# Optimization experiments

Hardware: AMD Instinct MI355X
Metric: run time of the kernel (lower is better)

The kernel has to match this reference:

```python
import jax, jax.numpy as jnp
import numpy as np

EPS = 1e-5

def _layernorm(h, g, b):
    mu = jnp.mean(h, axis=-1, keepdims=True)
    var = jnp.var(h, axis=-1, keepdims=True)
    return (h - mu) * jax.lax.rsqrt(var + EPS) * g + b

def setup_inputs() -> dict:
    key = jax.random.key(0)
    ks = jax.random.split(key, 12)
    N, D, E = 100000, 128, 1000000
    dims = [2 * D, 256, 128]  # [256, 256, 128]
    def lin(k, din, dout):
        s = 1.0 / np.sqrt(din)
        k1, k2 = jax.random.split(k)
        W = jax.random.uniform(k1, (din, dout), jnp.float32, -s, s)
        b = jax.random.uniform(k2, (dout,), jnp.float32, -s, s)
        return W, b
    x = jax.random.normal(ks[0], (N, D), jnp.float32)
    edge_index = jax.random.randint(ks[1], (2, E), 0, N, jnp.int32)
    w1, b1 = lin(ks[2], dims[0], dims[1])
    w2, b2 = lin(ks[3], dims[1], dims[2])
    wp, bp = lin(ks[4], dims[2], 1)
    ww, bw = lin(ks[5], dims[2], 1)
    return {
        "x": x, "edge_index": edge_index,
        "ln0_g": jnp.ones((dims[0],), jnp.float32), "ln0_b": jnp.zeros((dims[0],), jnp.float32),
        "w1": w1, "b1": b1,
        "ln1_g": jnp.ones((dims[1],), jnp.float32), "ln1_b": jnp.zeros((dims[1],), jnp.float32),
        "w2": w2, "b2": b2,
        "ln2_g": jnp.ones((dims[2],), jnp.float32), "ln2_b": jnp.zeros((dims[2],), jnp.float32),
        "wp": wp, "bp": bp, "ww": ww, "bw": bw,
    }

def reference(x, edge_index, ln0_g, ln0_b, w1, b1, ln1_g, ln1_b, w2, b2, ln2_g, ln2_b, wp, bp, ww, bw):
    src = x[edge_index[0]]          # [E, D] gather
    dst = x[edge_index[1]]          # [E, D] gather
    feats = jnp.concatenate([src + dst, src * dst], axis=-1)  # [E, 2D]
    h = _layernorm(feats, ln0_g, ln0_b)
    h = jax.nn.relu(_layernorm(h @ w1 + b1, ln1_g, ln1_b))
    h = jax.nn.relu(_layernorm(h @ w2 + b2, ln2_g, ln2_b))
    edge_probabilities = h @ wp + bp            # logits, [E, 1]
    edge_weights = jax.nn.relu(h @ ww + bw)     # [E, 1]
    return edge_probabilities, edge_weights
```

## Files before the change

kernel.cpp:

```cpp
#include <hip/hip_runtime.h>

#define EPS 1e-5f
#define PITCH 528

typedef __attribute__((ext_vector_type(8))) _Float16 f16x8;
typedef __attribute__((ext_vector_type(4))) _Float16 f16x4v;
typedef __attribute__((ext_vector_type(2))) _Float16 f16x2v;
typedef __attribute__((ext_vector_type(16))) float f32x16;

__global__ __launch_bounds__(256) void prep_x(const float* __restrict__ x,
                                              _Float16* __restrict__ x16, long n)
{
    const long i = ((long)blockIdx.x * 256 + threadIdx.x) * 8;
    if (i + 7 < n) {
        const float4 a = *reinterpret_cast<const float4*>(&x[i]);
        const float4 b = *reinterpret_cast<const float4*>(&x[i + 4]);
        f16x8 v;
        v[0] = (_Float16)a.x; v[1] = (_Float16)a.y; v[2] = (_Float16)a.z; v[3] = (_Float16)a.w;
        v[4] = (_Float16)b.x; v[5] = (_Float16)b.y; v[6] = (_Float16)b.z; v[7] = (_Float16)b.w;
        *reinterpret_cast<f16x8*>(&x16[i]) = v;
    }
}

__global__ __launch_bounds__(256) void prep_weights(
    const float* __restrict__ w1, const float* __restrict__ w2,
    _Float16* __restrict__ wb1, _Float16* __restrict__ wb2)
{
    const int t = blockIdx.x * 256 + threadIdx.x;
    const int lane = t & 63, frag = t >> 6;
    _Float16 v[8];
    if (frag < 128) {
        const int row0 = (frag & 15) * 16 + (lane >> 5) * 8;
        const int col = (frag >> 4) * 32 + (lane & 31);
        #pragma unroll
        for (int j = 0; j < 8; ++j) v[j] = (_Float16)w1[(row0 + j) * 256 + col];
        *reinterpret_cast<f16x8*>(&wb1[frag * 512 + lane * 8]) = *reinterpret_cast<f16x8*>(v);
    } else if (frag < 192) {
        const int f = frag - 128;
        const int row0 = (f & 15) * 16 + (lane >> 5) * 8;
        const int col = (f >> 4) * 32 + (lane & 31);
        #pragma unroll
        for (int j = 0; j < 8; ++j) v[j] = (_Float16)w2[(row0 + j) * 128 + col];
        *reinterpret_cast<f16x8*>(&wb2[f * 512 + lane * 8]) = *reinterpret_cast<f16x8*>(v);
    }
}

template<bool X16>
__global__ __launch_bounds__(1024, 4) void edge_mlp(
    const float* __restrict__ x, const _Float16* __restrict__ x16,
    const int* __restrict__ ei,
    const float* __restrict__ ln0_g, const float* __restrict__ ln0_b,
    const _Float16* __restrict__ wb1, const float* __restrict__ b1,
    const float* __restrict__ ln1_g, const float* __restrict__ ln1_b,
    const _Float16* __restrict__ wb2, const float* __restrict__ b2,
    const float* __restrict__ ln2_g, const float* __restrict__ ln2_b,
    const float* __restrict__ wp, const float* __restrict__ bp,
    const float* __restrict__ ww, const float* __restrict__ bw,
    float* __restrict__ out, int E)
{
    __shared__ __align__(16) _Float16 hh[128 * 264 + 8192];
    __shared__ __align__(8) float red[16][64][2];
    __shared__ __align__(8) float red2[16][32][2];

    const int tid = threadIdx.x, lane = tid & 63, w = tid >> 6;
    const int l31 = lane & 31, lh = lane >> 5;
    const int ft = w >> 1, ep = w & 1;
    const int ft2 = w >> 2, et2 = w & 3;
    const long base = (long)blockIdx.x * 128;

    {
        int si = 0;
        if (lane < 16) {
            const long idx = base + w * 8 + (lane >> 1);
            const int s = lane & 1;
            si = (idx < E) ? ei[(long)s * E + idx] : 0;
        }
        const int c = 2 * lane;
        const float ga = ln0_g[c], gb = ln0_g[c + 1], gc = ln0_g[128 + c], gd = ln0_g[129 + c];
        const float ba = ln0_b[c], bb = ln0_b[c + 1], bc = ln0_b[128 + c], bd = ln0_b[129 + c];
        char* hhc = (char*)hh;
        #pragma unroll
        for (int e8 = 0; e8 < 8; ++e8) {
            const int s0 = __shfl(si, e8 * 2 + 0);
            const int s1 = __shfl(si, e8 * 2 + 1);
            const int e = w * 8 + e8;
            float2 sv, dv;
            if constexpr (X16) {
                const f16x2v a2 = *reinterpret_cast<const f16x2v*>(&x16[(long)s0 * 128 + c]);
                const f16x2v d2 = *reinterpret_cast<const f16x2v*>(&x16[(long)s1 * 128 + c]);
                sv.x = (float)a2[0]; sv.y = (float)a2[1];
                dv.x = (float)d2[0]; dv.y = (float)d2[1];
            } else {
                sv = *reinterpret_cast<const float2*>(&x[(long)s0 * 128 + c]);
                dv = *reinterpret_cast<const float2*>(&x[(long)s1 * 128 + c]);
            }
            const float a0 = sv.x + dv.x, a1 = sv.y + dv.y;
            const float m0 = sv.x * dv.x, m1 = sv.y * dv.y;
            float s = a0 + a1 + m0 + m1;
            float q = a0 * a0 + a1 * a1 + m0 * m0 + m1 * m1;
            #pragma unroll
            for (int o = 32; o; o >>= 1) { s += __shfl_xor(s, o); q += __shfl_xor(q, o); }
            const float mu = s * (1.f / 256.f);
            const float rs = rsqrtf(q * (1.f / 256.f) - mu * mu + EPS);
            f16x2v p0, p1;
            p0[0] = (_Float16)((a0 - mu) * rs * ga + ba);
            p0[1] = (_Float16)((a1 - mu) * rs * gb + bb);
            p1[0] = (_Float16)((m0 - mu) * rs * gc + bc);
            p1[1] = (_Float16)((m1 - mu) * rs * gd + bd);
            const int o0 = e * PITCH + 4 * lane;
            const int o1 = e * PITCH + 256 + 4 * lane;
            *reinterpret_cast<f16x2v*>(hhc + o0) = p0;
            *reinterpret_cast<f16x2v*>(hhc + o1) = p1;
        }
    }
    __syncthreads();

    f32x16 acc1[2] = {};
    {
        const char* hhc = (const char*)hh;
        const int boffA = (ep * 64 + l31) * PITCH + lh * 16;
        const int boffB = (ep * 64 + 32 + l31) * PITCH + lh * 16;
        for (int ks = 0; ks < 16; ++ks) {
            const f16x8 a = *reinterpret_cast<const f16x8*>(&wb1[(ft * 16 + ks) * 512 + lane * 8]);
            const f16x8 bA = *reinterpret_cast<const f16x8*>(hhc + boffA + ks * 32);
            acc1[0] = __builtin_amdgcn_mfma_f32_32x32x16_f16(a, bA, acc1[0], 0, 0, 0);
            const f16x8 bB = *reinterpret_cast<const f16x8*>(hhc + boffB + ks * 32);
            acc1[1] = __builtin_amdgcn_mfma_f32_32x32x16_f16(a, bB, acc1[1], 0, 0, 0);
        }
        float bi[4][4];
        #pragma unroll
        for (int g2 = 0; g2 < 4; ++g2)
            *reinterpret_cast<float4*>(bi[g2]) =
                *reinterpret_cast<const float4*>(&b1[ft * 32 + g2 * 8 + 4 * lh]);
        #pragma unroll
        for (int t = 0; t < 2; ++t) {
            float s = 0.f, q = 0.f;
            #pragma unroll
            for (int r = 0; r < 16; ++r) {
                const float v2 = acc1[t][r] + bi[r >> 2][r & 3];
                acc1[t][r] = v2; s += v2; q += v2 * v2;
            }
            s += __shfl_xor(s, 32); q += __shfl_xor(q, 32);
            if (lane < 32) { red[w][t * 32 + lane][0] = s; red[w][t * 32 + lane][1] = q; }
        }
    }
    __syncthreads();

    {
        char* hhc = (char*)hh;
        #pragma unroll
        for (int t = 0; t < 2; ++t) {
            const int el = t * 32 + l31;
            const int e1 = ep * 64 + el;
            float S = 0.f, Q = 0.f;
            #pragma unroll
            for (int f = 0; f < 8; ++f) { S += red[2 * f + ep][el][0]; Q += red[2 * f + ep][el][1]; }
            const float mu = S * (1.f / 256.f);
            const float rs = rsqrtf(Q * (1.f / 256.f) - mu * mu + EPS);
            #pragma unroll
            for (int g2 = 0; g2 < 4; ++g2) {
                const int f0 = ft * 32 + g2 * 8 + 4 * lh;
                float gv[4], bv[4];
                *reinterpret_cast<float4*>(gv) = *reinterpret_cast<const float4*>(&ln1_g[f0]);
                *reinterpret_cast<float4*>(bv) = *reinterpret_cast<const float4*>(&ln1_b[f0]);
                f16x4v pk;
                #pragma unroll
                for (int ii = 0; ii < 4; ++ii)
                    pk[ii] = (_Float16)fmaxf((acc1[t][g2 * 4 + ii] - mu) * rs * gv[ii] + bv[ii], 0.f);
                *reinterpret_cast<f16x4v*>(hhc + e1 * PITCH + f0 * 2) = pk;
            }
        }
    }
    __syncthreads();

    f32x16 acc2 = {};
    {
        const char* hhc = (const char*)hh;
        const int e2 = et2 * 32 + l31;
        const int boff2 = e2 * PITCH + lh * 16;
        for (int ks = 0; ks < 16; ++ks) {
            const f16x8 a = *reinterpret_cast<const f16x8*>(&wb2[(ft2 * 16 + ks) * 512 + lane * 8]);
            const f16x8 b = *reinterpret_cast<const f16x8*>(hhc + boff2 + ks * 32);
            acc2 = __builtin_amdgcn_mfma_f32_32x32x16_f16(a, b, acc2, 0, 0, 0);
        }
        float bi[4][4];
        #pragma unroll
        for (int g2 = 0; g2 < 4; ++g2)
            *reinterpret_cast<float4*>(bi[g2]) =
                *reinterpret_cast<const float4*>(&b2[ft2 * 32 + g2 * 8 + 4 * lh]);
        float s = 0.f, q = 0.f;
        #pragma unroll
        for (int r = 0; r < 16; ++r) {
            const float v2 = acc2[r] + bi[r >> 2][r & 3];
            acc2[r] = v2; s += v2; q += v2 * v2;
        }
        s += __shfl_xor(s, 32); q += __shfl_xor(q, 32);
        if (lane < 32) { red[w][lane][0] = s; red[w][lane][1] = q; }
    }
    __syncthreads();

    {
        float S = 0.f, Q = 0.f;
        #pragma unroll
        for (int f2 = 0; f2 < 4; ++f2) { S += red[4 * f2 + et2][l31][0]; Q += red[4 * f2 + et2][l31][1]; }
        const float mu = S * (1.f / 128.f);
        const float rs = rsqrtf(Q * (1.f / 128.f) - mu * mu + EPS);
        float pp = 0.f, ws2 = 0.f;
        #pragma unroll
        for (int g2 = 0; g2 < 4; ++g2) {
            const int f0 = ft2 * 32 + g2 * 8 + 4 * lh;
            float gv[4], bv[4], pv[4], wv[4];
            *reinterpret_cast<float4*>(gv) = *reinterpret_cast<const float4*>(&ln2_g[f0]);
            *reinterpret_cast<float4*>(bv) = *reinterpret_cast<const float4*>(&ln2_b[f0]);
            *reinterpret_cast<float4*>(pv) = *reinterpret_cast<const float4*>(&wp[f0]);
            *reinterpret_cast<float4*>(wv) = *reinterpret_cast<const float4*>(&ww[f0]);
            #pragma unroll
            for (int ii = 0; ii < 4; ++ii) {
                const float t = fmaxf((acc2[g2 * 4 + ii] - mu) * rs * gv[ii] + bv[ii], 0.f);
                pp += t * pv[ii]; ws2 += t * wv[ii];
            }
        }
        pp += __shfl_xor(pp, 32); ws2 += __shfl_xor(ws2, 32);
        if (lane < 32) { red2[w][lane][0] = pp; red2[w][lane][1] = ws2; }
    }
    __syncthreads();

    if (tid < 128 && base + tid < E) {
        const int q5 = tid >> 5, l = tid & 31;
        float P = bp[0], W = bw[0];
        #pragma unroll
        for (int f2 = 0; f2 < 4; ++f2) { P += red2[4 * f2 + q5][l][0]; W += red2[4 * f2 + q5][l][1]; }
        out[base + tid] = P;
        out[(long)E + base + tid] = fmaxf(W, 0.f);
    }
}

extern "C" void kernel_launch(void* const* d_in, const int* in_sizes, int n_in,
                              void* d_out, int out_size, void* d_ws, size_t ws_size,
                              hipStream_t stream) {
    const float* x     = (const float*)d_in[0];
    const int*   ei    = (const int*)  d_in[1];
    const float* ln0_g = (const float*)d_in[2];
    const float* ln0_b = (const float*)d_in[3];
    const float* w1    = (const float*)d_in[4];
    const float* b1    = (const float*)d_in[5];
    const float* ln1_g = (const float*)d_in[6];
    const float* ln1_b = (const float*)d_in[7];
    const float* w2    = (const float*)d_in[8];
    const float* b2    = (const float*)d_in[9];
    const float* ln2_g = (const float*)d_in[10];
    const float* ln2_b = (const float*)d_in[11];
    const float* wp    = (const float*)d_in[12];
    const float* bp    = (const float*)d_in[13];
    const float* ww    = (const float*)d_in[14];
    const float* bw    = (const float*)d_in[15];

    _Float16* wb1 = (_Float16*)d_ws;
    _Float16* wb2 = wb1 + 128 * 512;
    _Float16* x16 = wb2 + 64 * 512;

    const int E = in_sizes[1] / 2;
    const long xN = (long)in_sizes[0];
    const size_t need = 192 * 1024 + (size_t)xN * sizeof(_Float16);

    prep_weights<<<48, 256, 0, stream>>>(w1, w2, wb1, wb2);
    if (ws_size >= need) {
        const int nb = (int)((xN / 8 + 255) / 256);
        prep_x<<<nb, 256, 0, stream>>>(x, x16, xN);
        edge_mlp<true><<<(E + 127) / 128, 1024, 0, stream>>>(
            x, x16, ei, ln0_g, ln0_b, wb1, b1, ln1_g, ln1_b, wb2, b2,
            ln2_g, ln2_b, wp, bp, ww, bw, (float*)d_out, E);
    } else {
        edge_mlp<false><<<(E + 127) / 128, 1024, 0, stream>>>(
            x, x16, ei, ln0_g, ln0_b, wb1, b1, ln1_g, ln1_b, wb2, b2,
            ln2_g, ln2_b, wp, bp, ww, bw, (float*)d_out, E);
    }
}
```

Baseline: 576.3 us.

## Process 256 edges per block to reuse weight fragments across more MFMA tiles

Doubles the per-block edge tile from 128 to 256, so each wave issues 4 (layer 1) and 2 (layer 2) MFMAs per loaded weight fragment instead of 2 and 1. This halves global weight-fragment loads per edge and halves the number of blocks. In exchange, shared memory grows to about 135 KB per block and more accumulator registers are live. Occupancy drops to one 1024-thread block per CU, which weakens latency hiding for the random gathers.

```diff
diff --git a/kernel.cpp b/kernel.cpp
--- a/kernel.cpp
+++ b/kernel.cpp
@@ -58,20 +58,20 @@
     const float* __restrict__ ww, const float* __restrict__ bw,
     float* __restrict__ out, int E)
 {
-    __shared__ __align__(16) _Float16 hh[128 * 264 + 8192];
-    __shared__ __align__(8) float red[16][64][2];
-    __shared__ __align__(8) float red2[16][32][2];
+    __shared__ __align__(16) _Float16 hh[256 * 264];
+    __shared__ __align__(8) float red[16][128][2];
+    __shared__ __align__(8) float red2[16][64][2];
 
     const int tid = threadIdx.x, lane = tid & 63, w = tid >> 6;
     const int l31 = lane & 31, lh = lane >> 5;
     const int ft = w >> 1, ep = w & 1;
-    const int ft2 = w >> 2, et2 = w & 3;
-    const long base = (long)blockIdx.x * 128;
+    const int ft2 = w >> 2, eq = w & 3;
+    const long base = (long)blockIdx.x * 256;
 
     {
         int si = 0;
-        if (lane < 16) {
-            const long idx = base + w * 8 + (lane >> 1);
+        if (lane < 32) {
+            const long idx = base + w * 16 + (lane >> 1);
             const int s = lane & 1;
             si = (idx < E) ? ei[(long)s * E + idx] : 0;
         }
@@ -80,10 +80,10 @@
         const float ba = ln0_b[c], bb = ln0_b[c + 1], bc = ln0_b[128 + c], bd = ln0_b[129 + c];
         char* hhc = (char*)hh;
         #pragma unroll
-        for (int e8 = 0; e8 < 8; ++e8) {
+        for (int e8 = 0; e8 < 16; ++e8) {
             const int s0 = __shfl(si, e8 * 2 + 0);
             const int s1 = __shfl(si, e8 * 2 + 1);
-            const int e = w * 8 + e8;
+            const int e = w * 16 + e8;
             float2 sv, dv;
             if constexpr (X16) {
                 const f16x2v a2 = *reinterpret_cast<const f16x2v*>(&x16[(long)s0 * 128 + c]);
@@ -115,17 +115,19 @@
     }
     __syncthreads();
 
-    f32x16 acc1[2] = {};
+    f32x16 acc1[4] = {};
     {
         const char* hhc = (const char*)hh;
-        const int boffA = (ep * 64 + l31) * PITCH + lh * 16;
-        const int boffB = (ep * 64 + 32 + l31) * PITCH + lh * 16;
+        int boff[4];
+        #pragma unroll
+        for (int t = 0; t < 4; ++t) boff[t] = (ep * 128 + t * 32 + l31) * PITCH + lh * 16;
         for (int ks = 0; ks < 16; ++ks) {
             const f16x8 a = *reinterpret_cast<const f16x8*>(&wb1[(ft * 16 + ks) * 512 + lane * 8]);
-            const f16x8 bA = *reinterpret_cast<const f16x8*>(hhc + boffA + ks * 32);
-            acc1[0] = __builtin_amdgcn_mfma_f32_32x32x16_f16(a, bA, acc1[0], 0, 0, 0);
-            const f16x8 bB = *reinterpret_cast<const f16x8*>(hhc + boffB + ks * 32);
-            acc1[1] = __builtin_amdgcn_mfma_f32_32x32x16_f16(a, bB, acc1[1], 0, 0, 0);
+            #pragma unroll
+            for (int t = 0; t < 4; ++t) {
+                const f16x8 b = *reinterpret_cast<const f16x8*>(hhc + boff[t] + ks * 32);
+                acc1[t] = __builtin_amdgcn_mfma_f32_32x32x16_f16(a, b, acc1[t], 0, 0, 0);
+            }
         }
         float bi[4][4];
         #pragma unroll
@@ -133,7 +135,7 @@
             *reinterpret_cast<float4*>(bi[g2]) =
                 *reinterpret_cast<const float4*>(&b1[ft * 32 + g2 * 8 + 4 * lh]);
         #pragma unroll
-        for (int t = 0; t < 2; ++t) {
+        for (int t = 0; t < 4; ++t) {
             float s = 0.f, q = 0.f;
             #pragma unroll
             for (int r = 0; r < 16; ++r) {
@@ -149,9 +151,9 @@
     {
         char* hhc = (char*)hh;
         #pragma unroll
-        for (int t = 0; t < 2; ++t) {
+        for (int t = 0; t < 4; ++t) {
             const int el = t * 32 + l31;
-            const int e1 = ep * 64 + el;
+            const int e1 = ep * 128 + el;
             float S = 0.f, Q = 0.f;
             #pragma unroll
             for (int f = 0; f < 8; ++f) { S += red[2 * f + ep][el][0]; Q += red[2 * f + ep][el][1]; }
@@ -173,63 +175,81 @@
     }
     __syncthreads();
 
-    f32x16 acc2 = {};
+    f32x16 acc2[2] = {};
     {
         const char* hhc = (const char*)hh;
-        const int e2 = et2 * 32 + l31;
-        const int boff2 = e2 * PITCH + lh * 16;
+        int boff2[2];
+        #pragma unroll
+        for (int ntl = 0; ntl < 2; ++ntl)
+            boff2[ntl] = ((2 * eq + ntl) * 32 + l31) * PITCH + lh * 16;
         for (int ks = 0; ks < 16; ++ks) {
             const f16x8 a = *reinterpret_cast<const f16x8*>(&wb2[(ft2 * 16 + ks) * 512 + lane * 8]);
-            const f16x8 b = *reinterpret_cast<const f16x8*>(hhc + boff2 + ks * 32);
-            acc2 = __builtin_amdgcn_mfma_f32_32x32x16_f16(a, b, acc2, 0, 0, 0);
+            #pragma unroll
+            for (int ntl = 0; ntl < 2; ++ntl) {
+                const f16x8 b = *reinterpret_cast<const f16x8*>(hhc + boff2[ntl] + ks * 32);
+                acc2[ntl] = __builtin_amdgcn_mfma_f32_32x32x16_f16(a, b, acc2[ntl], 0, 0, 0);
+            }
         }
         float bi[4][4];
         #pragma unroll
         for (int g2 = 0; g2 < 4; ++g2)
             *reinterpret_cast<float4*>(bi[g2]) =
                 *reinterpret_cast<const float4*>(&b2[ft2 * 32 + g2 * 8 + 4 * lh]);
-        float s = 0.f, q = 0.f;
-        #pragma unroll
-        for (int r = 0; r < 16; ++r) {
-            const float v2 = acc2[r] + bi[r >> 2][r & 3];
-            acc2[r] = v2; s += v2; q += v2 * v2;
-        }
-        s += __shfl_xor(s, 32); q += __shfl_xor(q, 32);
-        if (lane < 32) { red[w][lane][0] = s; red[w][lane][1] = q; }
-    }
-    __syncthreads();
-
-    {
-        float S = 0.f, Q = 0.f;
-        #pragma unroll
-        for (int f2 = 0; f2 < 4; ++f2) { S += red[4 * f2 + et2][l31][0]; Q += red[4 * f2 + et2][l31][1]; }
-        const float mu = S * (1.f / 128.f);
-        const float rs = rsqrtf(Q * (1.f / 128.f) - mu * mu + EPS);
-        float pp = 0.f, ws2 = 0.f;
-        #pragma unroll
-        for (int g2 = 0; g2 < 4; ++g2) {
-            const int f0 = ft2 * 32 + g2 * 8 + 4 * lh;
-            float gv[4], bv[4], pv[4], wv[4];
-            *reinterpret_cast<float4*>(gv) = *reinterpret_cast<const float4*>(&ln2_g[f0]);
-            *reinterpret_cast<float4*>(bv) = *reinterpret_cast<const float4*>(&ln2_b[f0]);
-            *reinterpret_cast<float4*>(pv) = *reinterpret_cast<const float4*>(&wp[f0]);
-            *reinterpret_cast<float4*>(wv) = *reinterpret_cast<const float4*>(&ww[f0]);
-            #pragma unroll
-            for (int ii = 0; ii < 4; ++ii) {
-                const float t = fmaxf((acc2[g2 * 4 + ii] - mu) * rs * gv[ii] + bv[ii], 0.f);
-                pp += t * pv[ii]; ws2 += t * wv[ii];
-            }
-        }
-        pp += __shfl_xor(pp, 32); ws2 += __shfl_xor(ws2, 32);
-        if (lane < 32) { red2[w][lane][0] = pp; red2[w][lane][1] = ws2; }
-    }
-    __syncthreads();
-
-    if (tid < 128 && base + tid < E) {
-        const int q5 = tid >> 5, l = tid & 31;
+        #pragma unroll
+        for (int ntl = 0; ntl < 2; ++ntl) {
+            float s = 0.f, q = 0.f;
+            #pragma unroll
+            for (int r = 0; r < 16; ++r) {
+                const float v2 = acc2[ntl][r] + bi[r >> 2][r & 3];
+                acc2[ntl][r] = v2; s += v2; q += v2 * v2;
+            }
+            s += __shfl_xor(s, 32); q += __shfl_xor(q, 32);
+            if (lane < 32) { red[w][ntl * 32 + lane][0] = s; red[w][ntl * 32 + lane][1] = q; }
+        }
+    }
+    __syncthreads();
+
+    {
+        #pragma unroll
+        for (int ntl = 0; ntl < 2; ++ntl) {
+            float S = 0.f, Q = 0.f;
+            #pragma unroll
+            for (int f2 = 0; f2 < 4; ++f2) {
+                S += red[f2 * 4 + eq][ntl * 32 + l31][0];
+                Q += red[f2 * 4 + eq][ntl * 32 + l31][1];
+            }
+            const float mu = S * (1.f / 128.f);
+            const float rs = rsqrtf(Q * (1.f / 128.f) - mu * mu + EPS);
+            float pp = 0.f, ws2 = 0.f;
+            #pragma unroll
+            for (int g2 = 0; g2 < 4; ++g2) {
+                const int f0 = ft2 * 32 + g2 * 8 + 4 * lh;
+                float gv[4], bv[4], pv[4], wv[4];
+                *reinterpret_cast<float4*>(gv) = *reinterpret_cast<const float4*>(&ln2_g[f0]);
+                *reinterpret_cast<float4*>(bv) = *reinterpret_cast<const float4*>(&ln2_b[f0]);
+                *reinterpret_cast<float4*>(pv) = *reinterpret_cast<const float4*>(&wp[f0]);
+                *reinterpret_cast<float4*>(wv) = *reinterpret_cast<const float4*>(&ww[f0]);
+                #pragma unroll
+                for (int ii = 0; ii < 4; ++ii) {
+                    const float t = fmaxf((acc2[ntl][g2 * 4 + ii] - mu) * rs * gv[ii] + bv[ii], 0.f);
+                    pp += t * pv[ii]; ws2 += t * wv[ii];
+                }
+            }
+            pp += __shfl_xor(pp, 32); ws2 += __shfl_xor(ws2, 32);
+            if (lane < 32) { red2[w][ntl * 32 + l31][0] = pp; red2[w][ntl * 32 + l31][1] = ws2; }
+        }
+    }
+    __syncthreads();
+
+    if (tid < 256 && base + tid < E) {
+        const int tile = tid >> 5, l = tid & 31;
+        const int eqo = tile >> 1, ntl = tile & 1;
         float P = bp[0], W = bw[0];
         #pragma unroll
-        for (int f2 = 0; f2 < 4; ++f2) { P += red2[4 * f2 + q5][l][0]; W += red2[4 * f2 + q5][l][1]; }
+        for (int f2 = 0; f2 < 4; ++f2) {
+            P += red2[f2 * 4 + eqo][ntl * 32 + l][0];
+            W += red2[f2 * 4 + eqo][ntl * 32 + l][1];
+        }
         out[base + tid] = P;
         out[(long)E + base + tid] = fmaxf(W, 0.f);
     }
@@ -267,11 +287,11 @@
     if (ws_size >= need) {
         const int nb = (int)((xN / 8 + 255) / 256);
         prep_x<<<nb, 256, 0, stream>>>(x, x16, xN);
-        edge_mlp<true><<<(E + 127) / 128, 1024, 0, stream>>>(
+        edge_mlp<true><<<(E + 255) / 256, 1024, 0, stream>>>(
             x, x16, ei, ln0_g, ln0_b, wb1, b1, ln1_g, ln1_b, wb2, b2,
             ln2_g, ln2_b, wp, bp, ww, bw, (float*)d_out, E);
     } else {
-        edge_mlp<false><<<(E + 127) / 128, 1024, 0, stream>>>(
+        edge_mlp<false><<<(E + 255) / 256, 1024, 0, stream>>>(
             x, x16, ei, ln0_g, ln0_b, wb1, b1, ln1_g, ln1_b, wb2, b2,
             ln2_g, ln2_b, wp, bp, ww, bw, (float*)d_out, E);
     }
```

New measurement: 666.4 us. 1.16x slower.
